# Performance work log

Measured on AMD Instinct MI355X. Metric: run time of the kernel, lower is better.

The kernel has to match this reference:

```python
import jax, jax.numpy as jnp
import numpy as np

BATCH, DIM, M, T = 256, 256, 64, 256
NUM_ITERS = 4
ZERO_HEAD = 16  # first 16 entries of U are zero (unweighted low-freq coeffs)


def setup_inputs() -> dict:
    key = jax.random.key(0)
    k1, k2, k3 = jax.random.split(key, 3)
    y = jax.random.normal(k1, (BATCH, DIM, T), dtype=jnp.float32)
    # small-norm measurement matrix so spectral radius of S stays < 1
    A = 0.02 * jax.random.normal(k2, (M, DIM), dtype=jnp.float32)
    # near-identity dictionary (trained D stays well-conditioned)
    D = jnp.eye(DIM, dtype=jnp.float32) + 0.02 * jax.random.normal(k3, (DIM, DIM), dtype=jnp.float32)
    F = jnp.eye(DIM, dtype=jnp.float32)
    lam1 = jnp.float32(0.5)
    lam2 = jnp.float32(1.0)
    alpha = jnp.float32(1.0)
    h0 = jnp.zeros((DIM,), dtype=jnp.float32)
    U = jnp.ones((DIM,), dtype=jnp.float32).at[:ZERO_HEAD].set(0.0)
    return {"y": y, "A": A, "D": D, "F": F, "lam1": lam1, "lam2": lam2,
            "alpha": alpha, "h0": h0, "U": U}


def _soft_threshold(z, U, b):
    # sign(z) * relu(|z| - U*b)
    return jnp.sign(z) * jnp.maximum(jnp.abs(z) - U * b, 0.0)


def reference(y, A, D, F, lam1, lam2, alpha, h0, U):
    dim = D.shape[0]
    I = jnp.eye(dim, dtype=D.dtype)
    P = D.T @ F @ D                                      # (dim, dim)
    S = I - (1.0 / alpha) * (D.T @ (A.T @ A + lam2 * I) @ D)  # (dim, dim)
    V = (1.0 / alpha) * (D.T @ A.T)                      # (dim, m)
    x = jnp.einsum('md,bdt->tbm', A, y)                  # measurements, (T, B, m)
    b = lam1 / alpha
    c2 = lam2 / alpha

    def step(h_pre, x_t):
        # h_pre: (B, dim), x_t: (B, m)
        Ph = h_pre @ P.T                                 # (B, dim)
        const = x_t @ V.T + c2 * Ph                      # (B, dim), fixed over inner iters
        h_t = Ph
        for _ in range(NUM_ITERS):
            h_t = _soft_threshold(h_t @ S.T + const, U, b)
        return h_t, h_t

    h_init = jnp.broadcast_to(h0, (y.shape[0], dim))
    _, hs = jax.lax.scan(step, h_init, x)                # hs: (T, B, dim)
    h = jnp.transpose(hs, (1, 2, 0))                     # (B, dim, T)
    return jnp.einsum('nd,bdt->bnt', D, h)               # y_re: (B, dim, T)
```

## Files before the change

kernel.cpp:

```cpp
#include <hip/hip_runtime.h>
#include <hip/hip_bf16.h>

typedef unsigned int u32;
typedef unsigned short u16;

#define DIMN 256
#define TLEN 256

typedef _Float16 half2v __attribute__((ext_vector_type(2)));
typedef _Float16 f16x8  __attribute__((ext_vector_type(8)));
typedef float    f32x4  __attribute__((ext_vector_type(4)));

__device__ __forceinline__ u32 packh2(float lo, float hi) {
    _Float16 l = (_Float16)lo, h = (_Float16)hi;
    u16 lu = __builtin_bit_cast(u16, l);
    u16 hu = __builtin_bit_cast(u16, h);
    return (u32)lu | ((u32)hu << 16);
}

__device__ __forceinline__ float h2lo(u32 v) {
    return (float)__builtin_bit_cast(half2v, v).x;
}
__device__ __forceinline__ float h2hi(u32 v) {
    return (float)__builtin_bit_cast(half2v, v).y;
}

__global__ void prep1(const float* __restrict__ A, const float* __restrict__ D,
                      const float* __restrict__ F, const float* __restrict__ lam2p,
                      float* __restrict__ FD, float* __restrict__ G,
                      float* __restrict__ AD) {
    int gid = blockIdx.x * 256 + threadIdx.x;
    if (gid < 65536) {
        int k = gid >> 8, j = gid & 255;
        float s = 0.f;
        #pragma unroll 8
        for (int q = 0; q < 256; ++q) s += F[k*256+q] * D[q*256+j];
        FD[gid] = s;
    } else if (gid < 131072) {
        int g = gid - 65536; int p = g >> 8, q = g & 255;
        float s = (p == q) ? lam2p[0] : 0.f;
        #pragma unroll 8
        for (int m = 0; m < 64; ++m) s += A[m*256+p] * A[m*256+q];
        G[g] = s;
    } else if (gid < 147456) {
        int g = gid - 131072; int m = g >> 8, i = g & 255;
        float s = 0.f;
        #pragma unroll 8
        for (int k = 0; k < 256; ++k) s += A[m*256+k] * D[k*256+i];
        AD[g] = s;
    }
}

__global__ void prep2(const float* __restrict__ A, const float* __restrict__ D,
                      const float* __restrict__ alphap,
                      const float* __restrict__ FD, const float* __restrict__ G,
                      const float* __restrict__ AD,
                      float* __restrict__ Pt, float* __restrict__ GD,
                      float* __restrict__ Wt) {
    int gid = blockIdx.x * 256 + threadIdx.x;
    float inva = 1.0f / alphap[0];
    if (gid < 65536) {
        int j = gid >> 8, i = gid & 255;
        float s = 0.f;
        #pragma unroll 8
        for (int k = 0; k < 256; ++k) s += D[k*256+i] * FD[k*256+j];
        Pt[gid] = s;
    } else if (gid < 131072) {
        int g = gid - 65536; int k = g >> 8, j = g & 255;
        float s = 0.f;
        #pragma unroll 8
        for (int q = 0; q < 256; ++q) s += G[k*256+q] * D[q*256+j];
        GD[g] = s;
    } else {
        int g = gid - 131072; int d = g >> 8, i = g & 255;
        float s = 0.f;
        #pragma unroll 8
        for (int m = 0; m < 64; ++m) s += AD[m*256+i] * A[m*256+d];
        Wt[g] = inva * s;
    }
}

__global__ void prep3(const float* __restrict__ D, const float* __restrict__ GD,
                      const float* __restrict__ alphap, float* __restrict__ St) {
    int gid = blockIdx.x * 256 + threadIdx.x;
    int j = gid >> 8, i = gid & 255;
    float inva = 1.0f / alphap[0];
    float s = 0.f;
    #pragma unroll 8
    for (int k = 0; k < 256; ++k) s += D[k*256+i] * GD[k*256+j];
    St[gid] = ((i == j) ? 1.0f : 0.0f) - inva * s;
}

__global__ void prep5(const float* __restrict__ St, const float* __restrict__ Pt,
                      const float* __restrict__ lam2p, const float* __restrict__ alphap,
                      float* __restrict__ Qt) {
    int gid = blockIdx.x * 256 + threadIdx.x;
    int j = gid >> 8, i = gid & 255;
    float c2 = lam2p[0] / alphap[0];
    float s = c2 * Pt[j*256 + i];
    #pragma unroll 8
    for (int k = 0; k < 256; ++k) s += St[k*256+i] * Pt[j*256+k];
    Qt[gid] = s;
}

__global__ void prep4(const float* __restrict__ St, const float* __restrict__ Pt,
                      const float* __restrict__ Qt, const float* __restrict__ Wt,
                      u32* __restrict__ Sfrag, u32* __restrict__ Pfrag,
                      u32* __restrict__ Qfrag, u32* __restrict__ Wfrag) {
    int gid = blockIdx.x * 256 + threadIdx.x;
    int sel = gid >> 13;
    int idx = gid & 8191;
    int l   = idx & 63;
    int kk  = (idx >> 6) & 7;
    int tau = idx >> 9;
    int row = 16*tau + (l & 15);
    int k0  = 32*kk + 8*(l >> 4);
    const float* M = (sel == 0) ? St : (sel == 1) ? Pt : (sel == 2) ? Qt : Wt;
    u32* O = (sel == 0) ? Sfrag : (sel == 1) ? Pfrag : (sel == 2) ? Qfrag : Wfrag;
    uint4 v;
    v.x = packh2(M[(k0+0)*256 + row], M[(k0+1)*256 + row]);
    v.y = packh2(M[(k0+2)*256 + row], M[(k0+3)*256 + row]);
    v.z = packh2(M[(k0+4)*256 + row], M[(k0+5)*256 + row]);
    v.w = packh2(M[(k0+6)*256 + row], M[(k0+7)*256 + row]);
    *(uint4*)&O[idx*4] = v;
}

__global__ void prep6(const float* __restrict__ D, u32* __restrict__ Dfrag) {
    int idx = blockIdx.x * 256 + threadIdx.x;
    int l   = idx & 63;
    int kk  = (idx >> 6) & 7;
    int tau = idx >> 9;
    int row = 16*tau + (l & 15);
    int k0  = 32*kk + 8*(l >> 4);
    float4 fa = *(const float4*)&D[row*256 + k0];
    float4 fb = *(const float4*)&D[row*256 + k0 + 4];
    uint4 v;
    v.x = packh2(fa.x, fa.y);
    v.y = packh2(fa.z, fa.w);
    v.z = packh2(fb.x, fb.y);
    v.w = packh2(fb.z, fb.w);
    *(uint4*)&Dfrag[idx*4] = v;
}

__global__ __attribute__((amdgpu_flat_work_group_size(512, 512),
                          amdgpu_waves_per_eu(2)))
void zgemm2(const float* __restrict__ y, const u32* __restrict__ Wfrag,
            u32* __restrict__ Zh) {
    __shared__ u32 yl[16384];
    const int tid = threadIdx.x;
    const int l   = tid & 63;
    const int w   = tid >> 6;
    const int g   = l >> 4;
    const int c   = l & 15;
    const int b   = blockIdx.x;
    const int t0  = blockIdx.y * 128;

    #pragma unroll
    for (int it = 0; it < 8; ++it) {
        int idx = it * 512 + tid;
        int dp = idx >> 5;
        int tq = idx & 31;
        const float* yb = y + ((size_t)b*256 + 2*dp)*256 + t0 + 4*tq;
        float4 fa = *(const float4*)yb;
        float4 fb = *(const float4*)(yb + 256);
        const float* fav = (const float*)&fa;
        const float* fbv = (const float*)&fb;
        #pragma unroll
        for (int j = 0; j < 4; ++j) {
            int tl = 4*tq + j;
            yl[tl*128 + (dp ^ ((tl & 7) << 2))] = packh2(fav[j], fbv[j]);
        }
    }

    f16x8 Wf0[8], Wf1[8];
    #pragma unroll
    for (int kk = 0; kk < 8; ++kk) {
        Wf0[kk] = __builtin_bit_cast(f16x8, *(const uint4*)&Wfrag[(((2*w+0)*8 + kk)*64 + l)*4]);
        Wf1[kk] = __builtin_bit_cast(f16x8, *(const uint4*)&Wfrag[(((2*w+1)*8 + kk)*64 + l)*4]);
    }
    __syncthreads();

    f32x4 acc0[8], acc1[8];
    #pragma unroll
    for (int tt = 0; tt < 8; ++tt) {
        acc0[tt] = (f32x4){0.f,0.f,0.f,0.f};
        acc1[tt] = (f32x4){0.f,0.f,0.f,0.f};
    }
    const int swz = (c & 7) << 2;
    #pragma unroll
    for (int tt = 0; tt < 8; ++tt) {
        const int tl = 16*tt + c;
        #pragma unroll
        for (int kk = 0; kk < 8; ++kk) {
            int idx = tl*128 + ((16*kk + 4*g) ^ swz);
            f16x8 bf = __builtin_bit_cast(f16x8, *(const uint4*)&yl[idx]);
            acc0[tt] = __builtin_amdgcn_mfma_f32_16x16x32_f16(Wf0[kk], bf, acc0[tt], 0, 0, 0);
            acc1[tt] = __builtin_amdgcn_mfma_f32_16x16x32_f16(Wf1[kk], bf, acc1[tt], 0, 0, 0);
        }
    }
    #pragma unroll
    for (int tt = 0; tt < 8; ++tt) {
        const int t = t0 + 16*tt + c;
        uint2 p0, p1;
        p0.x = packh2(acc0[tt][0], acc0[tt][1]);
        p0.y = packh2(acc0[tt][2], acc0[tt][3]);
        p1.x = packh2(acc1[tt][0], acc1[tt][1]);
        p1.y = packh2(acc1[tt][2], acc1[tt][3]);
        u32* zp = &Zh[((size_t)(b*256 + t))*128 + 16*w + 2*g];
        *(uint2*)(zp)     = p0;
        *(uint2*)(zp + 8) = p1;
    }
}

__global__ __attribute__((amdgpu_flat_work_group_size(512, 512),
                          amdgpu_waves_per_eu(2, 2)))
void scan9(const u32* __restrict__ Sfrag, const u32* __restrict__ Pfrag,
           const u32* __restrict__ Qfrag,
           const u32* __restrict__ Zh,
           const float* __restrict__ h0, const float* __restrict__ U,
           const float* __restrict__ lam1p, const float* __restrict__ lam2p,
           const float* __restrict__ alphap,
           u32* __restrict__ Hh) {
    __shared__ __align__(16) u32 hx[2 * 2048];

    const int tid = threadIdx.x;
    const int l   = tid & 63;
    const int w   = tid >> 6;
    const int lb  = l & 15;
    const int g   = l >> 4;
    const int b   = blockIdx.x * 16 + lb;

    const float inva = 1.0f / alphap[0];
    const float bt   = lam1p[0] * inva;
    const float c2   = lam2p[0] * inva;

    const int rb = 32*w + 4*g;
    const float u00 = U[rb+0]*bt,  u01 = U[rb+1]*bt,  u02 = U[rb+2]*bt,  u03 = U[rb+3]*bt;
    const float u10 = U[rb+16]*bt, u11 = U[rb+17]*bt, u12 = U[rb+18]*bt, u13 = U[rb+19]*bt;

    f16x8 Sf0[8], Sf1[8], Pf0[8], Pf1[8], Qf0[8], Qf1[8];
    #pragma unroll
    for (int kk = 0; kk < 8; ++kk) {
        Sf0[kk] = __builtin_bit_cast(f16x8, *(const uint4*)&Sfrag[(((2*w+0)*8 + kk)*64 + l)*4]);
        Sf1[kk] = __builtin_bit_cast(f16x8, *(const uint4*)&Sfrag[(((2*w+1)*8 + kk)*64 + l)*4]);
        Pf0[kk] = __builtin_bit_cast(f16x8, *(const uint4*)&Pfrag[(((2*w+0)*8 + kk)*64 + l)*4]);
        Pf1[kk] = __builtin_bit_cast(f16x8, *(const uint4*)&Pfrag[(((2*w+1)*8 + kk)*64 + l)*4]);
        Qf0[kk] = __builtin_bit_cast(f16x8, *(const uint4*)&Qfrag[(((2*w+0)*8 + kk)*64 + l)*4]);
        Qf1[kk] = __builtin_bit_cast(f16x8, *(const uint4*)&Qfrag[(((2*w+1)*8 + kk)*64 + l)*4]);
    }

    {
        int k0 = 32*(tid >> 6) + 8*((tid & 63) >> 4);
        uint4 hv;
        hv.x = packh2(h0[k0+0], h0[k0+1]);
        hv.y = packh2(h0[k0+2], h0[k0+3]);
        hv.z = packh2(h0[k0+4], h0[k0+5]);
        hv.w = packh2(h0[k0+6], h0[k0+7]);
        *(uint4*)&hx[tid*4] = hv;
    }
    __syncthreads();

    const u32* Zb = Zh + (size_t)b*32768 + 16*w + 2*g;
    u32* Hbh = Hh + (size_t)b*32768 + 16*w + 2*g;

    const int wb0 = w*256 + (((g>>1))*16 + lb)*4 + (g&1)*2;

    uint2 z0 = *(const uint2*)&Zb[0];
    uint2 z1 = *(const uint2*)&Zb[8];

    #pragma unroll 1
    for (int t = 0; t < TLEN; ++t) {
        f16x8 hb[8];
        #pragma unroll
        for (int kk = 0; kk < 8; ++kk)
            hb[kk] = __builtin_bit_cast(f16x8, *(const uint4*)&hx[0 + (kk*64 + l)*4]);
        f32x4 q0 = {h2lo(z0.x), h2hi(z0.x), h2lo(z0.y), h2hi(z0.y)};
        f32x4 q1 = {h2lo(z1.x), h2hi(z1.x), h2lo(z1.y), h2hi(z1.y)};
        f32x4 a0 = {0.f,0.f,0.f,0.f}, a1 = {0.f,0.f,0.f,0.f};
        #pragma unroll
        for (int kk = 0; kk < 8; ++kk) {
            q0 = __builtin_amdgcn_mfma_f32_16x16x32_f16(Qf0[kk], hb[kk], q0, 0, 0, 0);
            q1 = __builtin_amdgcn_mfma_f32_16x16x32_f16(Qf1[kk], hb[kk], q1, 0, 0, 0);
            a0 = __builtin_amdgcn_mfma_f32_16x16x32_f16(Pf0[kk], hb[kk], a0, 0, 0, 0);
            a1 = __builtin_amdgcn_mfma_f32_16x16x32_f16(Pf1[kk], hb[kk], a1, 0, 0, 0);
        }
        {
            const float h00 = copysignf(fmaxf(fabsf(q0[0]) - u00, 0.f), q0[0]);
            const float h01 = copysignf(fmaxf(fabsf(q0[1]) - u01, 0.f), q0[1]);
            const float h02 = copysignf(fmaxf(fabsf(q0[2]) - u02, 0.f), q0[2]);
            const float h03 = copysignf(fmaxf(fabsf(q0[3]) - u03, 0.f), q0[3]);
            const float h10 = copysignf(fmaxf(fabsf(q1[0]) - u10, 0.f), q1[0]);
            const float h11 = copysignf(fmaxf(fabsf(q1[1]) - u11, 0.f), q1[1]);
            const float h12 = copysignf(fmaxf(fabsf(q1[2]) - u12, 0.f), q1[2]);
            const float h13 = copysignf(fmaxf(fabsf(q1[3]) - u13, 0.f), q1[3]);
            *(uint2*)&hx[2048 + wb0]       = make_uint2(packh2(h00,h01), packh2(h02,h03));
            *(uint2*)&hx[2048 + wb0 + 128] = make_uint2(packh2(h10,h11), packh2(h12,h13));
        }
        __syncthreads();

        const int tn = (t < TLEN-1) ? t + 1 : t;
        uint2 zn0 = *(const uint2*)&Zb[(size_t)tn*128];
        uint2 zn1 = *(const uint2*)&Zb[(size_t)tn*128 + 8];

        const float c00 = h2lo(z0.x) + c2*a0[0];
        const float c01 = h2hi(z0.x) + c2*a0[1];
        const float c02 = h2lo(z0.y) + c2*a0[2];
        const float c03 = h2hi(z0.y) + c2*a0[3];
        const float c10 = h2lo(z1.x) + c2*a1[0];
        const float c11 = h2hi(z1.x) + c2*a1[1];
        const float c12 = h2lo(z1.y) + c2*a1[2];
        const float c13 = h2hi(z1.y) + c2*a1[3];

        #pragma unroll
        for (int it = 0; it < 3; ++it) {
            const int rd = (it & 1) ? 0 : 2048;
            const int wr = (it & 1) ? 2048 : 0;
            #pragma unroll
            for (int kk = 0; kk < 8; ++kk)
                hb[kk] = __builtin_bit_cast(f16x8, *(const uint4*)&hx[rd + (kk*64 + l)*4]);
            f32x4 s0 = {c00,c01,c02,c03};
            f32x4 s1 = {c10,c11,c12,c13};
            #pragma unroll
            for (int kk = 0; kk < 8; ++kk) {
                s0 = __builtin_amdgcn_mfma_f32_16x16x32_f16(Sf0[kk], hb[kk], s0, 0, 0, 0);
                s1 = __builtin_amdgcn_mfma_f32_16x16x32_f16(Sf1[kk], hb[kk], s1, 0, 0, 0);
            }
            const float h00 = copysignf(fmaxf(fabsf(s0[0]) - u00, 0.f), s0[0]);
            const float h01 = copysignf(fmaxf(fabsf(s0[1]) - u01, 0.f), s0[1]);
            const float h02 = copysignf(fmaxf(fabsf(s0[2]) - u02, 0.f), s0[2]);
            const float h03 = copysignf(fmaxf(fabsf(s0[3]) - u03, 0.f), s0[3]);
            const float h10 = copysignf(fmaxf(fabsf(s1[0]) - u10, 0.f), s1[0]);
            const float h11 = copysignf(fmaxf(fabsf(s1[1]) - u11, 0.f), s1[1]);
            const float h12 = copysignf(fmaxf(fabsf(s1[2]) - u12, 0.f), s1[2]);
            const float h13 = copysignf(fmaxf(fabsf(s1[3]) - u13, 0.f), s1[3]);
            *(uint2*)&hx[wr + wb0]       = make_uint2(packh2(h00,h01), packh2(h02,h03));
            *(uint2*)&hx[wr + wb0 + 128] = make_uint2(packh2(h10,h11), packh2(h12,h13));
            __syncthreads();
            if (it == 2) {
                *(uint2*)&Hbh[(size_t)t*128]     = make_uint2(packh2(h00,h01), packh2(h02,h03));
                *(uint2*)&Hbh[(size_t)t*128 + 8] = make_uint2(packh2(h10,h11), packh2(h12,h13));
            }
        }
        z0 = zn0; z1 = zn1;
    }
}

__global__ __attribute__((amdgpu_flat_work_group_size(512, 512),
                          amdgpu_waves_per_eu(2)))
void ogemm2(const u32* __restrict__ Dfrag, const u32* __restrict__ Hh,
            float* __restrict__ out) {
    __shared__ u32 hl[16384];
    const int tid = threadIdx.x;
    const int l   = tid & 63;
    const int w   = tid >> 6;
    const int g   = l >> 4;
    const int c   = l & 15;
    const int b   = blockIdx.x;
    const int t0  = blockIdx.y * 128;

    const uint4* Hg = (const uint4*)(Hh + (size_t)b*32768 + (size_t)t0*128);
    #pragma unroll
    for (int it = 0; it < 8; ++it) {
        int j4 = it * 512 + tid;
        int tl = j4 >> 5, m = j4 & 31;
        ((uint4*)hl)[tl*32 + (m ^ (tl & 7))] = Hg[j4];
    }

    f16x8 Df0[8], Df1[8];
    #pragma unroll
    for (int kk = 0; kk < 8; ++kk) {
        Df0[kk] = __builtin_bit_cast(f16x8, *(const uint4*)&Dfrag[(((2*w+0)*8 + kk)*64 + l)*4]);
        Df1[kk] = __builtin_bit_cast(f16x8, *(const uint4*)&Dfrag[(((2*w+1)*8 + kk)*64 + l)*4]);
    }
    __syncthreads();

    f32x4 acc0[8], acc1[8];
    #pragma unroll
    for (int tt = 0; tt < 8; ++tt) {
        acc0[tt] = (f32x4){0.f,0.f,0.f,0.f};
        acc1[tt] = (f32x4){0.f,0.f,0.f,0.f};
    }
    const int swz = (c & 7) << 2;
    #pragma unroll
    for (int tt = 0; tt < 8; ++tt) {
        const int tl = 16*tt + c;
        #pragma unroll
        for (int kk = 0; kk < 8; ++kk) {
            int idx = tl*128 + ((16*kk + 4*g) ^ swz);
            f16x8 bf = __builtin_bit_cast(f16x8, *(const uint4*)&hl[idx]);
            acc0[tt] = __builtin_amdgcn_mfma_f32_16x16x32_f16(Df0[kk], bf, acc0[tt], 0, 0, 0);
            acc1[tt] = __builtin_amdgcn_mfma_f32_16x16x32_f16(Df1[kk], bf, acc1[tt], 0, 0, 0);
        }
    }
    #pragma unroll
    for (int tt = 0; tt < 8; ++tt) {
        const int t = t0 + 16*tt + c;
        const int n0 = 16*(2*w+0) + 4*g;
        const int n1 = 16*(2*w+1) + 4*g;
        #pragma unroll
        for (int r = 0; r < 4; ++r) {
            out[((size_t)(b*256) + n0 + r)*256 + t] = acc0[tt][r];
            out[((size_t)(b*256) + n1 + r)*256 + t] = acc1[tt][r];
        }
    }
}

extern "C" void kernel_launch(void* const* d_in, const int* in_sizes, int n_in,
                              void* d_out, int out_size, void* d_ws, size_t ws_size,
                              hipStream_t stream) {
    const float* y     = (const float*)d_in[0];
    const float* A     = (const float*)d_in[1];
    const float* D     = (const float*)d_in[2];
    const float* F     = (const float*)d_in[3];
    const float* lam1  = (const float*)d_in[4];
    const float* lam2  = (const float*)d_in[5];
    const float* alpha = (const float*)d_in[6];
    const float* h0    = (const float*)d_in[7];
    const float* U     = (const float*)d_in[8];
    float* out = (float*)d_out;
    float* ws  = (float*)d_ws;

    const size_t oZ  = 0;
    const size_t oH  = 16777216;
    const size_t oWt = 33554432;
    const size_t oSt = 33619968;
    const size_t oPt = 33685504;
    const size_t oFD = 33751040;
    const size_t oG  = 33816576;
    const size_t oGD = 33882112;
    const size_t oAD = 33947648;
    const size_t oSh = 33964032;
    const size_t oPh = 33996800;

    u32*   Zh = (u32*)(ws + oZ);
    u32*   Hh = (u32*)(ws + oH);
    float* Wt = ws + oWt; float* St = ws + oSt; float* Pt = ws + oPt;
    float* FD = ws + oFD; float* G  = ws + oG;  float* GD = ws + oGD;
    float* AD = ws + oAD;
    float* Qt = ws + oFD;
    u32* Sfrag = (u32*)(ws + oSh);
    u32* Pfrag = (u32*)(ws + oPh);
    u32* Qfrag = (u32*)(ws + oG);
    u32* Wfrag = (u32*)(ws + oGD);
    u32* Dfrag = (u32*)(ws + oGD + 32768);

    prep1<<<576, 256, 0, stream>>>(A, D, F, lam2, FD, G, AD);
    prep2<<<768, 256, 0, stream>>>(A, D, alpha, FD, G, AD, Pt, GD, Wt);
    prep3<<<256, 256, 0, stream>>>(D, GD, alpha, St);
    prep5<<<256, 256, 0, stream>>>(St, Pt, lam2, alpha, Qt);
    prep4<<<128, 256, 0, stream>>>(St, Pt, Qt, Wt, Sfrag, Pfrag, Qfrag, Wfrag);
    prep6<<<32, 256, 0, stream>>>(D, Dfrag);
    {
        dim3 gz(256, 2);
        zgemm2<<<gz, 512, 0, stream>>>(y, Wfrag, Zh);
    }
    scan9<<<16, 512, 0, stream>>>(Sfrag, Pfrag, Qfrag, Zh, h0, U, lam1, lam2, alpha, Hh);
    {
        dim3 go(256, 2);
        ogemm2<<<go, 512, 0, stream>>>(Dfrag, Hh, out);
    }
}
```

Baseline: 789.6 us.

## Drop precomputed Q matrix, run four plain S iterations with 4-wave scan blocks

The scan no longer uses the fused Q = S·P + c2·P matrix to do the first inner iteration. It computes Ph once, then runs all four S iterations explicitly, which removes the prep5 kernel and the Q fragments. Each workgroup now has 4 waves instead of 8, and each wave handles 4 row tiles whose S and P fragments are held in registers. This cuts barrier participants and merges the prep6 packing into prep4, at the cost of more serial MFMA work per wave and high register pressure.

```diff
diff --git a/kernel.cpp b/kernel.cpp
--- a/kernel.cpp
+++ b/kernel.cpp
@@ -91,22 +91,10 @@
     St[gid] = ((i == j) ? 1.0f : 0.0f) - inva * s;
 }
 
-__global__ void prep5(const float* __restrict__ St, const float* __restrict__ Pt,
-                      const float* __restrict__ lam2p, const float* __restrict__ alphap,
-                      float* __restrict__ Qt) {
-    int gid = blockIdx.x * 256 + threadIdx.x;
-    int j = gid >> 8, i = gid & 255;
-    float c2 = lam2p[0] / alphap[0];
-    float s = c2 * Pt[j*256 + i];
-    #pragma unroll 8
-    for (int k = 0; k < 256; ++k) s += St[k*256+i] * Pt[j*256+k];
-    Qt[gid] = s;
-}
-
 __global__ void prep4(const float* __restrict__ St, const float* __restrict__ Pt,
-                      const float* __restrict__ Qt, const float* __restrict__ Wt,
+                      const float* __restrict__ Wt, const float* __restrict__ Dm,
                       u32* __restrict__ Sfrag, u32* __restrict__ Pfrag,
-                      u32* __restrict__ Qfrag, u32* __restrict__ Wfrag) {
+                      u32* __restrict__ Wfrag, u32* __restrict__ Dfrag) {
     int gid = blockIdx.x * 256 + threadIdx.x;
     int sel = gid >> 13;
     int idx = gid & 8191;
@@ -115,31 +103,24 @@
     int tau = idx >> 9;
     int row = 16*tau + (l & 15);
     int k0  = 32*kk + 8*(l >> 4);
-    const float* M = (sel == 0) ? St : (sel == 1) ? Pt : (sel == 2) ? Qt : Wt;
-    u32* O = (sel == 0) ? Sfrag : (sel == 1) ? Pfrag : (sel == 2) ? Qfrag : Wfrag;
     uint4 v;
+    if (sel == 3) {
+        float4 fa = *(const float4*)&Dm[row*256 + k0];
+        float4 fb = *(const float4*)&Dm[row*256 + k0 + 4];
+        v.x = packh2(fa.x, fa.y);
+        v.y = packh2(fa.z, fa.w);
+        v.z = packh2(fb.x, fb.y);
+        v.w = packh2(fb.z, fb.w);
+        *(uint4*)&Dfrag[idx*4] = v;
+        return;
+    }
+    const float* M = (sel == 0) ? St : (sel == 1) ? Pt : Wt;
+    u32* O = (sel == 0) ? Sfrag : (sel == 1) ? Pfrag : Wfrag;
     v.x = packh2(M[(k0+0)*256 + row], M[(k0+1)*256 + row]);
     v.y = packh2(M[(k0+2)*256 + row], M[(k0+3)*256 + row]);
     v.z = packh2(M[(k0+4)*256 + row], M[(k0+5)*256 + row]);
     v.w = packh2(M[(k0+6)*256 + row], M[(k0+7)*256 + row]);
     *(uint4*)&O[idx*4] = v;
-}
-
-__global__ void prep6(const float* __restrict__ D, u32* __restrict__ Dfrag) {
-    int idx = blockIdx.x * 256 + threadIdx.x;
-    int l   = idx & 63;
-    int kk  = (idx >> 6) & 7;
-    int tau = idx >> 9;
-    int row = 16*tau + (l & 15);
-    int k0  = 32*kk + 8*(l >> 4);
-    float4 fa = *(const float4*)&D[row*256 + k0];
-    float4 fb = *(const float4*)&D[row*256 + k0 + 4];
-    uint4 v;
-    v.x = packh2(fa.x, fa.y);
-    v.y = packh2(fa.z, fa.w);
-    v.z = packh2(fb.x, fb.y);
-    v.w = packh2(fb.z, fb.w);
-    *(uint4*)&Dfrag[idx*4] = v;
 }
 
 __global__ __attribute__((amdgpu_flat_work_group_size(512, 512),
@@ -212,15 +193,14 @@
     }
 }
 
-__global__ __attribute__((amdgpu_flat_work_group_size(512, 512),
-                          amdgpu_waves_per_eu(2, 2)))
-void scan9(const u32* __restrict__ Sfrag, const u32* __restrict__ Pfrag,
-           const u32* __restrict__ Qfrag,
-           const u32* __restrict__ Zh,
-           const float* __restrict__ h0, const float* __restrict__ U,
-           const float* __restrict__ lam1p, const float* __restrict__ lam2p,
-           const float* __restrict__ alphap,
-           u32* __restrict__ Hh) {
+__global__ __attribute__((amdgpu_flat_work_group_size(256, 256),
+                          amdgpu_waves_per_eu(1, 1)))
+void scan12(const u32* __restrict__ Sfrag, const u32* __restrict__ Pfrag,
+            const u32* __restrict__ Zh,
+            const float* __restrict__ h0, const float* __restrict__ U,
+            const float* __restrict__ lam1p, const float* __restrict__ lam2p,
+            const float* __restrict__ alphap,
+            u32* __restrict__ Hh) {
     __shared__ __align__(16) u32 hx[2 * 2048];
 
     const int tid = threadIdx.x;
@@ -234,114 +214,128 @@
     const float bt   = lam1p[0] * inva;
     const float c2   = lam2p[0] * inva;
 
-    const int rb = 32*w + 4*g;
-    const float u00 = U[rb+0]*bt,  u01 = U[rb+1]*bt,  u02 = U[rb+2]*bt,  u03 = U[rb+3]*bt;
-    const float u10 = U[rb+16]*bt, u11 = U[rb+17]*bt, u12 = U[rb+18]*bt, u13 = U[rb+19]*bt;
-
-    f16x8 Sf0[8], Sf1[8], Pf0[8], Pf1[8], Qf0[8], Qf1[8];
-    #pragma unroll
-    for (int kk = 0; kk < 8; ++kk) {
-        Sf0[kk] = __builtin_bit_cast(f16x8, *(const uint4*)&Sfrag[(((2*w+0)*8 + kk)*64 + l)*4]);
-        Sf1[kk] = __builtin_bit_cast(f16x8, *(const uint4*)&Sfrag[(((2*w+1)*8 + kk)*64 + l)*4]);
-        Pf0[kk] = __builtin_bit_cast(f16x8, *(const uint4*)&Pfrag[(((2*w+0)*8 + kk)*64 + l)*4]);
-        Pf1[kk] = __builtin_bit_cast(f16x8, *(const uint4*)&Pfrag[(((2*w+1)*8 + kk)*64 + l)*4]);
-        Qf0[kk] = __builtin_bit_cast(f16x8, *(const uint4*)&Qfrag[(((2*w+0)*8 + kk)*64 + l)*4]);
-        Qf1[kk] = __builtin_bit_cast(f16x8, *(const uint4*)&Qfrag[(((2*w+1)*8 + kk)*64 + l)*4]);
-    }
-
-    {
-        int k0 = 32*(tid >> 6) + 8*((tid & 63) >> 4);
+    float uu[4][4];
+    #pragma unroll
+    for (int T = 0; T < 4; ++T) {
+        int rb = 16*(4*w + T) + 4*g;
+        #pragma unroll
+        for (int r = 0; r < 4; ++r) uu[T][r] = U[rb + r] * bt;
+    }
+
+    f16x8 Sf[4][8], Pf[4][8];
+    #pragma unroll
+    for (int T = 0; T < 4; ++T) {
+        #pragma unroll
+        for (int kk = 0; kk < 8; ++kk) {
+            Sf[T][kk] = __builtin_bit_cast(f16x8, *(const uint4*)&Sfrag[(((4*w+T)*8 + kk)*64 + l)*4]);
+            Pf[T][kk] = __builtin_bit_cast(f16x8, *(const uint4*)&Pfrag[(((4*w+T)*8 + kk)*64 + l)*4]);
+        }
+    }
+
+    #pragma unroll
+    for (int ii = 0; ii < 2; ++ii) {
+        int idx = tid + 256*ii;
+        int k0 = 32*(idx >> 6) + 8*((idx & 63) >> 4);
         uint4 hv;
         hv.x = packh2(h0[k0+0], h0[k0+1]);
         hv.y = packh2(h0[k0+2], h0[k0+3]);
         hv.z = packh2(h0[k0+4], h0[k0+5]);
         hv.w = packh2(h0[k0+6], h0[k0+7]);
-        *(uint4*)&hx[tid*4] = hv;
+        *(uint4*)&hx[idx*4] = hv;
     }
     __syncthreads();
 
-    const u32* Zb = Zh + (size_t)b*32768 + 16*w + 2*g;
-    u32* Hbh = Hh + (size_t)b*32768 + 16*w + 2*g;
-
-    const int wb0 = w*256 + (((g>>1))*16 + lb)*4 + (g&1)*2;
-
-    uint2 z0 = *(const uint2*)&Zb[0];
-    uint2 z1 = *(const uint2*)&Zb[8];
+    const u32* Zb  = Zh + (size_t)b*32768 + 32*w + 2*g;
+    u32*       Hbh = Hh + (size_t)b*32768 + 32*w + 2*g;
+
+    int wslot[4];
+    #pragma unroll
+    for (int T = 0; T < 4; ++T)
+        wslot[T] = (2*w + (T >> 1))*256 + ((2*(T & 1) + (g >> 1))*16 + lb)*4 + (g & 1)*2;
+
+    uint2 z[4];
+    #pragma unroll
+    for (int T = 0; T < 4; ++T) z[T] = *(const uint2*)&Zb[8*T];
+
+    int ro = 0, wo = 2048;
 
     #pragma unroll 1
     for (int t = 0; t < TLEN; ++t) {
         f16x8 hb[8];
         #pragma unroll
         for (int kk = 0; kk < 8; ++kk)
-            hb[kk] = __builtin_bit_cast(f16x8, *(const uint4*)&hx[0 + (kk*64 + l)*4]);
-        f32x4 q0 = {h2lo(z0.x), h2hi(z0.x), h2lo(z0.y), h2hi(z0.y)};
-        f32x4 q1 = {h2lo(z1.x), h2hi(z1.x), h2lo(z1.y), h2hi(z1.y)};
-        f32x4 a0 = {0.f,0.f,0.f,0.f}, a1 = {0.f,0.f,0.f,0.f};
+            hb[kk] = __builtin_bit_cast(f16x8, *(const uint4*)&hx[ro + (kk*64 + l)*4]);
+        f32x4 a[4];
+        #pragma unroll
+        for (int T = 0; T < 4; ++T) a[T] = (f32x4){0.f,0.f,0.f,0.f};
         #pragma unroll
         for (int kk = 0; kk < 8; ++kk) {
-            q0 = __builtin_amdgcn_mfma_f32_16x16x32_f16(Qf0[kk], hb[kk], q0, 0, 0, 0);
-            q1 = __builtin_amdgcn_mfma_f32_16x16x32_f16(Qf1[kk], hb[kk], q1, 0, 0, 0);
-            a0 = __builtin_amdgcn_mfma_f32_16x16x32_f16(Pf0[kk], hb[kk], a0, 0, 0, 0);
-            a1 = __builtin_amdgcn_mfma_f32_16x16x32_f16(Pf1[kk], hb[kk], a1, 0, 0, 0);
-        }
-        {
-            const float h00 = copysignf(fmaxf(fabsf(q0[0]) - u00, 0.f), q0[0]);
-            const float h01 = copysignf(fmaxf(fabsf(q0[1]) - u01, 0.f), q0[1]);
-            const float h02 = copysignf(fmaxf(fabsf(q0[2]) - u02, 0.f), q0[2]);
-            const float h03 = copysignf(fmaxf(fabsf(q0[3]) - u03, 0.f), q0[3]);
-            const float h10 = copysignf(fmaxf(fabsf(q1[0]) - u10, 0.f), q1[0]);
-            const float h11 = copysignf(fmaxf(fabsf(q1[1]) - u11, 0.f), q1[1]);
-            const float h12 = copysignf(fmaxf(fabsf(q1[2]) - u12, 0.f), q1[2]);
-            const float h13 = copysignf(fmaxf(fabsf(q1[3]) - u13, 0.f), q1[3]);
-            *(uint2*)&hx[2048 + wb0]       = make_uint2(packh2(h00,h01), packh2(h02,h03));
-            *(uint2*)&hx[2048 + wb0 + 128] = make_uint2(packh2(h10,h11), packh2(h12,h13));
-        }
+            #pragma unroll
+            for (int T = 0; T < 4; ++T)
+                a[T] = __builtin_amdgcn_mfma_f32_16x16x32_f16(Pf[T][kk], hb[kk], a[T], 0, 0, 0);
+        }
+        #pragma unroll
+        for (int T = 0; T < 4; ++T)
+            *(uint2*)&hx[wo + wslot[T]] = make_uint2(packh2(a[T][0], a[T][1]),
+                                                     packh2(a[T][2], a[T][3]));
         __syncthreads();
 
         const int tn = (t < TLEN-1) ? t + 1 : t;
-        uint2 zn0 = *(const uint2*)&Zb[(size_t)tn*128];
-        uint2 zn1 = *(const uint2*)&Zb[(size_t)tn*128 + 8];
-
-        const float c00 = h2lo(z0.x) + c2*a0[0];
-        const float c01 = h2hi(z0.x) + c2*a0[1];
-        const float c02 = h2lo(z0.y) + c2*a0[2];
-        const float c03 = h2hi(z0.y) + c2*a0[3];
-        const float c10 = h2lo(z1.x) + c2*a1[0];
-        const float c11 = h2hi(z1.x) + c2*a1[1];
-        const float c12 = h2lo(z1.y) + c2*a1[2];
-        const float c13 = h2hi(z1.y) + c2*a1[3];
-
-        #pragma unroll
-        for (int it = 0; it < 3; ++it) {
-            const int rd = (it & 1) ? 0 : 2048;
-            const int wr = (it & 1) ? 2048 : 0;
+        uint2 zn[4];
+        #pragma unroll
+        for (int T = 0; T < 4; ++T) zn[T] = *(const uint2*)&Zb[(size_t)tn*128 + 8*T];
+
+        float cc[4][4];
+        #pragma unroll
+        for (int T = 0; T < 4; ++T) {
+            cc[T][0] = h2lo(z[T].x) + c2*a[T][0];
+            cc[T][1] = h2hi(z[T].x) + c2*a[T][1];
+            cc[T][2] = h2lo(z[T].y) + c2*a[T][2];
+            cc[T][3] = h2hi(z[T].y) + c2*a[T][3];
+        }
+        int rr = wo, ww = ro;
+
+        #pragma unroll
+        for (int it = 0; it < 4; ++it) {
             #pragma unroll
             for (int kk = 0; kk < 8; ++kk)
-                hb[kk] = __builtin_bit_cast(f16x8, *(const uint4*)&hx[rd + (kk*64 + l)*4]);
-            f32x4 s0 = {c00,c01,c02,c03};
-            f32x4 s1 = {c10,c11,c12,c13};
+                hb[kk] = __builtin_bit_cast(f16x8, *(const uint4*)&hx[rr + (kk*64 + l)*4]);
+            f32x4 s[4];
+            #pragma unroll
+            for (int T = 0; T < 4; ++T) s[T] = (f32x4){cc[T][0], cc[T][1], cc[T][2], cc[T][3]};
             #pragma unroll
             for (int kk = 0; kk < 8; ++kk) {
-                s0 = __builtin_amdgcn_mfma_f32_16x16x32_f16(Sf0[kk], hb[kk], s0, 0, 0, 0);
-                s1 = __builtin_amdgcn_mfma_f32_16x16x32_f16(Sf1[kk], hb[kk], s1, 0, 0, 0);
+                #pragma unroll
+                for (int T = 0; T < 4; ++T)
+                    s[T] = __builtin_amdgcn_mfma_f32_16x16x32_f16(Sf[T][kk], hb[kk], s[T], 0, 0, 0);
             }
-            const float h00 = copysignf(fmaxf(fabsf(s0[0]) - u00, 0.f), s0[0]);
-            const float h01 = copysignf(fmaxf(fabsf(s0[1]) - u01, 0.f), s0[1]);
-            const float h02 = copysignf(fmaxf(fabsf(s0[2]) - u02, 0.f), s0[2]);
-            const float h03 = copysignf(fmaxf(fabsf(s0[3]) - u03, 0.f), s0[3]);
-            const float h10 = copysignf(fmaxf(fabsf(s1[0]) - u10, 0.f), s1[0]);
-            const float h11 = copysignf(fmaxf(fabsf(s1[1]) - u11, 0.f), s1[1]);
-            const float h12 = copysignf(fmaxf(fabsf(s1[2]) - u12, 0.f), s1[2]);
-            const float h13 = copysignf(fmaxf(fabsf(s1[3]) - u13, 0.f), s1[3]);
-            *(uint2*)&hx[wr + wb0]       = make_uint2(packh2(h00,h01), packh2(h02,h03));
-            *(uint2*)&hx[wr + wb0 + 128] = make_uint2(packh2(h10,h11), packh2(h12,h13));
+            float hv[4][4];
+            #pragma unroll
+            for (int T = 0; T < 4; ++T) {
+                #pragma unroll
+                for (int r = 0; r < 4; ++r) {
+                    float v = s[T][r];
+                    float av = fabsf(v) - uu[T][r];
+                    hv[T][r] = (av > 0.f) ? copysignf(av, v) : 0.f;
+                }
+            }
+            uint2 pk[4];
+            #pragma unroll
+            for (int T = 0; T < 4; ++T) {
+                pk[T] = make_uint2(packh2(hv[T][0], hv[T][1]), packh2(hv[T][2], hv[T][3]));
+                *(uint2*)&hx[ww + wslot[T]] = pk[T];
+            }
             __syncthreads();
-            if (it == 2) {
-                *(uint2*)&Hbh[(size_t)t*128]     = make_uint2(packh2(h00,h01), packh2(h02,h03));
-                *(uint2*)&Hbh[(size_t)t*128 + 8] = make_uint2(packh2(h10,h11), packh2(h12,h13));
+            if (it == 3) {
+                #pragma unroll
+                for (int T = 0; T < 4; ++T)
+                    *(uint2*)&Hbh[(size_t)t*128 + 8*T] = pk[T];
             }
-        }
-        z0 = zn0; z1 = zn1;
+            int tmp = rr; rr = ww; ww = tmp;
+        }
+        ro = rr; wo = ww;
+        #pragma unroll
+        for (int T = 0; T < 4; ++T) z[T] = zn[T];
     }
 }
 
@@ -437,24 +431,20 @@
     float* Wt = ws + oWt; float* St = ws + oSt; float* Pt = ws + oPt;
     float* FD = ws + oFD; float* G  = ws + oG;  float* GD = ws + oGD;
     float* AD = ws + oAD;
-    float* Qt = ws + oFD;
     u32* Sfrag = (u32*)(ws + oSh);
     u32* Pfrag = (u32*)(ws + oPh);
-    u32* Qfrag = (u32*)(ws + oG);
     u32* Wfrag = (u32*)(ws + oGD);
     u32* Dfrag = (u32*)(ws + oGD + 32768);
 
     prep1<<<576, 256, 0, stream>>>(A, D, F, lam2, FD, G, AD);
     prep2<<<768, 256, 0, stream>>>(A, D, alpha, FD, G, AD, Pt, GD, Wt);
     prep3<<<256, 256, 0, stream>>>(D, GD, alpha, St);
-    prep5<<<256, 256, 0, stream>>>(St, Pt, lam2, alpha, Qt);
-    prep4<<<128, 256, 0, stream>>>(St, Pt, Qt, Wt, Sfrag, Pfrag, Qfrag, Wfrag);
-    prep6<<<32, 256, 0, stream>>>(D, Dfrag);
+    prep4<<<128, 256, 0, stream>>>(St, Pt, Wt, D, Sfrag, Pfrag, Wfrag, Dfrag);
     {
         dim3 gz(256, 2);
         zgemm2<<<gz, 512, 0, stream>>>(y, Wfrag, Zh);
     }
-    scan9<<<16, 512, 0, stream>>>(Sfrag, Pfrag, Qfrag, Zh, h0, U, lam1, lam2, alpha, Hh);
+    scan12<<<16, 256, 0, stream>>>(Sfrag, Pfrag, Zh, h0, U, lam1, lam2, alpha, Hh);
     {
         dim3 go(256, 2);
         ogemm2<<<go, 512, 0, stream>>>(Dfrag, Hh, out);
```

New measurement: 976.7 us. +23.7%, slower.
